# Optimization experiments

Measured on AMD Instinct MI355X. Metric: run time of the kernel, lower is better.

Reference implementation:

```python
import jax, jax.numpy as jnp
import numpy as np

COMMITMENT_COST = 0.25
NUM_EMBEDDINGS = 1024
EMBEDDING_DIM = 256


def setup_inputs() -> dict:
    key = jax.random.key(0)
    k1, k2 = jax.random.split(key)
    inputs = jax.random.normal(k1, (16, 4096, EMBEDDING_DIM), dtype=jnp.float32)
    # codebook initialized uniform(-1/K, 1/K) as in the torch module
    embeddings = jax.random.uniform(
        k2, (NUM_EMBEDDINGS, EMBEDDING_DIM), dtype=jnp.float32,
        minval=-1.0 / NUM_EMBEDDINGS, maxval=1.0 / NUM_EMBEDDINGS)
    return {"inputs": inputs, "embeddings": embeddings}


def reference(inputs, embeddings):
    sg = jax.lax.stop_gradient
    D = embeddings.shape[1]
    input_shape = inputs.shape
    flat = sg(inputs).reshape(-1, D)  # [N, D]
    distances = (jnp.sum(embeddings ** 2, axis=1)
                 + jnp.sum(flat ** 2, axis=1, keepdims=True)
                 - 2.0 * jnp.matmul(flat, embeddings.T))  # [N, K]
    indices = jnp.argmin(distances, axis=-1)  # [N]
    quantized = embeddings[indices].reshape(input_shape)
    e_latent_loss = jnp.mean((sg(quantized) - inputs) ** 2)
    q_latent_loss = jnp.mean((quantized - sg(inputs)) ** 2)
    loss = q_latent_loss + COMMITMENT_COST * e_latent_loss
    # straight-through estimator
    quantized = inputs + sg(quantized - inputs)
    return loss, quantized
```

## Files before the change

### kernel.cpp

```cpp
#include <hip/hip_runtime.h>
#include <math.h>

#define DIM 256
#define KCODES 1024
#define NTILE 64
#define BM 128
#define ESCALE 512.0f
#define UNIT_SCALE 0x7F7F7F7F

typedef __attribute__((ext_vector_type(8))) int i32x8;
typedef __attribute__((ext_vector_type(4))) float f32x4;

__global__ __launch_bounds__(64) void vq_prep_kernel(
    const float* __restrict__ E, float* __restrict__ enormh,
    unsigned char* __restrict__ Ef8) {
  const int k = blockIdx.x;
  const int t = threadIdx.x;
  const float4 v = *reinterpret_cast<const float4*>(&E[k * DIM + t * 4]);
  const int d0 = t * 4;
  const size_t byte = (size_t)((k >> 4) * 4096) + (size_t)((d0 >> 7) * 2048) +
                      (size_t)(((((d0 >> 5) & 3) * 16) + (k & 15)) * 32) +
                      (size_t)(d0 & 31);
  int p = __builtin_amdgcn_cvt_pk_fp8_f32(v.x * ESCALE, v.y * ESCALE, 0, 0);
  p = __builtin_amdgcn_cvt_pk_fp8_f32(v.z * ESCALE, v.w * ESCALE, p, 1);
  *reinterpret_cast<unsigned int*>(Ef8 + byte) = (unsigned int)p;
  float s = v.x * v.x + v.y * v.y + v.z * v.z + v.w * v.w;
#pragma unroll
  for (int off = 32; off >= 1; off >>= 1) s += __shfl_down(s, off);
  if (t == 0) enormh[k] = -0.5f * ESCALE * s;
}

__global__ __launch_bounds__(256, 2) void vq_fused_kernel(
    const float* __restrict__ X, const float* __restrict__ E,
    const unsigned char* __restrict__ Ef8, const float* __restrict__ enormh,
    float* __restrict__ outq, float* __restrict__ partials) {
  __shared__ __attribute__((aligned(16))) char ring[4][4][4096];
  __shared__ float enorm_s[KCODES];
  __shared__ int idxs[BM];
  __shared__ float lred[4];

  const int tid = threadIdx.x;
  const int w = tid >> 6;
  const int lane = tid & 63;
  const int lr = lane & 15;
  const int lk = lane >> 4;
  const int row0 = blockIdx.x * BM;

  {
    const float4 v = *reinterpret_cast<const float4*>(&enormh[tid * 4]);
    *reinterpret_cast<float4*>(&enorm_s[tid * 4]) = v;
  }

  i32x8 Af[2][2];
  float xsq = 0.0f;
#pragma unroll
  for (int mt = 0; mt < 2; ++mt) {
    const float* xrow = &X[(size_t)(row0 + w * 32 + mt * 16 + lr) * DIM];
#pragma unroll
    for (int ks2 = 0; ks2 < 2; ++ks2) {
      const int k0 = ks2 * 128 + lk * 32;
      i32x8 af;
#pragma unroll
      for (int p = 0; p < 8; ++p) {
        const float4 a = *reinterpret_cast<const float4*>(&xrow[k0 + p * 4]);
        xsq += a.x * a.x + a.y * a.y + a.z * a.z + a.w * a.w;
        int pk = __builtin_amdgcn_cvt_pk_fp8_f32(a.x, a.y, 0, 0);
        pk = __builtin_amdgcn_cvt_pk_fp8_f32(a.z, a.w, pk, 1);
        af[p] = pk;
      }
      Af[mt][ks2] = af;
    }
  }

  float maxv[8];
  int mini[8];
#pragma unroll
  for (int i = 0; i < 8; ++i) { maxv[i] = -INFINITY; mini[i] = 0; }

  const char* efsrc = reinterpret_cast<const char*>(Ef8) + lane * 16;
  char* ringw = &ring[w][0][0];

  __syncthreads();

#define ISSUE(T)                                                              \
  {                                                                           \
    const char* src_ = efsrc + (size_t)(T) * 4096;                            \
    char* dst_ = ringw + ((T) & 3) * 4096;                                    \
    _Pragma("unroll") for (int i_ = 0; i_ < 4; ++i_)                          \
        __builtin_amdgcn_global_load_lds(                                     \
            (const __attribute__((address_space(1))) unsigned int*)(src_ +    \
                                                                    i_ *      \
                                                                        1024),\
            (__attribute__((address_space(3))) unsigned int*)(dst_ +          \
                                                              i_ * 1024 +     \
                                                              lane * 16),     \
            16, 0, 0);                                                        \
  }

#define CONSUME(T)                                                            \
  {                                                                           \
    const char* cbuf_ = ringw + ((T) & 3) * 4096;                             \
    const float en_ = enorm_s[(T) * 16 + lr];                                 \
    const i32x8 b0_ = *reinterpret_cast<const i32x8*>(cbuf_ + lane * 32);     \
    const i32x8 b1_ =                                                         \
        *reinterpret_cast<const i32x8*>(cbuf_ + 2048 + lane * 32);            \
    f32x4 acc0, acc1;                                                         \
    acc0[0] = en_; acc0[1] = en_; acc0[2] = en_; acc0[3] = en_;               \
    acc1 = acc0;                                                              \
    acc0 = __builtin_amdgcn_mfma_scale_f32_16x16x128_f8f6f4(                  \
        Af[0][0], b0_, acc0, 0, 0, 0, UNIT_SCALE, 0, UNIT_SCALE);             \
    acc1 = __builtin_amdgcn_mfma_scale_f32_16x16x128_f8f6f4(                  \
        Af[1][0], b0_, acc1, 0, 0, 0, UNIT_SCALE, 0, UNIT_SCALE);             \
    acc0 = __builtin_amdgcn_mfma_scale_f32_16x16x128_f8f6f4(                  \
        Af[0][1], b1_, acc0, 0, 0, 0, UNIT_SCALE, 0, UNIT_SCALE);             \
    acc1 = __builtin_amdgcn_mfma_scale_f32_16x16x128_f8f6f4(                  \
        Af[1][1], b1_, acc1, 0, 0, 0, UNIT_SCALE, 0, UNIT_SCALE);             \
    const int code_ = (T) * 16 + lr;                                          \
    _Pragma("unroll") for (int r_ = 0; r_ < 4; ++r_) {                        \
      if (acc0[r_] > maxv[r_]) { maxv[r_] = acc0[r_]; mini[r_] = code_; }     \
      if (acc1[r_] > maxv[4 + r_]) {                                          \
        maxv[4 + r_] = acc1[r_]; mini[4 + r_] = code_;                        \
      }                                                                       \
    }                                                                         \
  }

  ISSUE(0);
  ISSUE(1);
  ISSUE(2);

#pragma unroll 4
  for (int t = 0; t < NTILE - 4; ++t) {
    ISSUE(t + 3);
    asm volatile("s_waitcnt vmcnt(12)" ::: "memory");
    __builtin_amdgcn_sched_barrier(0);
    CONSUME(t);
  }
  ISSUE(63);
  asm volatile("s_waitcnt vmcnt(12)" ::: "memory");
  __builtin_amdgcn_sched_barrier(0);
  CONSUME(60);
  asm volatile("s_waitcnt vmcnt(8)" ::: "memory");
  __builtin_amdgcn_sched_barrier(0);
  CONSUME(61);
  asm volatile("s_waitcnt vmcnt(4)" ::: "memory");
  __builtin_amdgcn_sched_barrier(0);
  CONSUME(62);
  asm volatile("s_waitcnt vmcnt(0)" ::: "memory");
  __builtin_amdgcn_sched_barrier(0);
  CONSUME(63);
#undef ISSUE
#undef CONSUME

#pragma unroll
  for (int off = 1; off < 16; off <<= 1) {
#pragma unroll
    for (int ri = 0; ri < 8; ++ri) {
      const float ov = __shfl_xor(maxv[ri], off);
      const int oi = __shfl_xor(mini[ri], off);
      if (ov > maxv[ri] || (ov == maxv[ri] && oi < mini[ri])) {
        maxv[ri] = ov; mini[ri] = oi;
      }
    }
  }
  if (lr == 0) {
#pragma unroll
    for (int mt = 0; mt < 2; ++mt)
#pragma unroll
      for (int r = 0; r < 4; ++r)
        idxs[w * 32 + mt * 16 + lk * 4 + r] = mini[mt * 4 + r];
  }

  float lsum = xsq;
  if (lr == 0) {
    float ssum = 0.0f;
#pragma unroll
    for (int ri = 0; ri < 8; ++ri) ssum += maxv[ri];
    lsum += ssum * (-2.0f / ESCALE);
  }
#pragma unroll
  for (int off = 32; off >= 1; off >>= 1) lsum += __shfl_down(lsum, off);
  if (lane == 0) lred[w] = lsum;
  __syncthreads();

#pragma unroll
  for (int half = 0; half < 2; ++half) {
    const int er = half * 64 + (tid >> 2);
    const int eq = tid & 3;
    const int code = idxs[er];
    const float* erow = &E[(size_t)code * DIM];
    float* orow = &outq[(size_t)(row0 + er) * DIM];
#pragma unroll
    for (int j = 0; j < 16; ++j) {
      const int d = j * 16 + eq * 4;
      *reinterpret_cast<float4*>(&orow[d]) =
          *reinterpret_cast<const float4*>(&erow[d]);
    }
  }
  if (tid == 0)
    partials[blockIdx.x] = lred[0] + lred[1] + lred[2] + lred[3];
}

__global__ __launch_bounds__(256) void vq_finalize_kernel(
    const float* __restrict__ partials, float* __restrict__ out_loss,
    int nparts, float inv_count) {
  const int tid = threadIdx.x;
  float s = 0.0f;
  for (int i = tid; i < nparts; i += 256) s += partials[i];
#pragma unroll
  for (int off = 32; off >= 1; off >>= 1) s += __shfl_down(s, off);
  __shared__ float w[4];
  if ((tid & 63) == 0) w[tid >> 6] = s;
  __syncthreads();
  if (tid == 0)
    out_loss[0] = 1.25f * (w[0] + w[1] + w[2] + w[3]) * inv_count;
}

extern "C" void kernel_launch(void* const* d_in, const int* in_sizes, int n_in,
                              void* d_out, int out_size, void* d_ws,
                              size_t ws_size, hipStream_t stream) {
  const float* X = (const float*)d_in[0];
  const float* E = (const float*)d_in[1];
  float* out = (float*)d_out;

  char* ws = (char*)d_ws;
  float* enormh = (float*)ws;
  float* partials = (float*)(ws + 16 * 1024);
  unsigned char* Ef8 = (unsigned char*)(ws + 48 * 1024);

  const int nrows = in_sizes[0] / DIM;
  const int nb_main = nrows / BM;

  vq_prep_kernel<<<KCODES, 64, 0, stream>>>(E, enormh, Ef8);
  vq_fused_kernel<<<nb_main, 256, 0, stream>>>(X, E, Ef8, enormh, out + 1,
                                               partials);
  vq_finalize_kernel<<<1, 256, 0, stream>>>(partials, out, nb_main,
                                            1.0f / (float)in_sizes[0]);
}
```

Measured before the change: 62.94 us.

## Load fp8 codebook tiles directly into registers instead of LDS ring

Drops the per-wave LDS ring buffer fed by global_load_lds and the shared enorm copy. The pre-swizzled fp8 codebook tiles and norms are now loaded straight from global (L2) into registers, double-buffered two tiles ahead, inside a fully unrolled loop. This removes LDS traffic, the block barrier and the manual waitcnt choreography, and frees LDS for higher occupancy. The cost is more VGPRs and reliance on the compiler's waitcnt placement to hide global latency with only two tiles of prefetch.

```diff
diff --git a/kernel.cpp b/kernel.cpp
--- a/kernel.cpp
+++ b/kernel.cpp
@@ -34,8 +34,6 @@
     const float* __restrict__ X, const float* __restrict__ E,
     const unsigned char* __restrict__ Ef8, const float* __restrict__ enormh,
     float* __restrict__ outq, float* __restrict__ partials) {
-  __shared__ __attribute__((aligned(16))) char ring[4][4][4096];
-  __shared__ float enorm_s[KCODES];
   __shared__ int idxs[BM];
   __shared__ float lred[4];
 
@@ -45,11 +43,6 @@
   const int lr = lane & 15;
   const int lk = lane >> 4;
   const int row0 = blockIdx.x * BM;
-
-  {
-    const float4 v = *reinterpret_cast<const float4*>(&enormh[tid * 4]);
-    *reinterpret_cast<float4*>(&enorm_s[tid * 4]) = v;
-  }
 
   i32x8 Af[2][2];
   float xsq = 0.0f;
@@ -77,79 +70,60 @@
 #pragma unroll
   for (int i = 0; i < 8; ++i) { maxv[i] = -INFINITY; mini[i] = 0; }
 
-  const char* efsrc = reinterpret_cast<const char*>(Ef8) + lane * 16;
-  char* ringw = &ring[w][0][0];
-
-  __syncthreads();
-
-#define ISSUE(T)                                                              \
+  const char* efbase = reinterpret_cast<const char*>(Ef8) + lane * 32;
+
+  i32x8 B0a, B0b, B1a, B1b;
+  float en0, en1;
+  B0a = *reinterpret_cast<const i32x8*>(efbase);
+  B0b = *reinterpret_cast<const i32x8*>(efbase + 2048);
+  B1a = *reinterpret_cast<const i32x8*>(efbase + 4096);
+  B1b = *reinterpret_cast<const i32x8*>(efbase + 4096 + 2048);
+  en0 = enormh[lr];
+  en1 = enormh[16 + lr];
+
+#define COMPUTE_TILE(BA, BB)                                                  \
   {                                                                           \
-    const char* src_ = efsrc + (size_t)(T) * 4096;                            \
-    char* dst_ = ringw + ((T) & 3) * 4096;                                    \
-    _Pragma("unroll") for (int i_ = 0; i_ < 4; ++i_)                          \
-        __builtin_amdgcn_global_load_lds(                                     \
-            (const __attribute__((address_space(1))) unsigned int*)(src_ +    \
-                                                                    i_ *      \
-                                                                        1024),\
-            (__attribute__((address_space(3))) unsigned int*)(dst_ +          \
-                                                              i_ * 1024 +     \
-                                                              lane * 16),     \
-            16, 0, 0);                                                        \
-  }
-
-#define CONSUME(T)                                                            \
+    acc0 = __builtin_amdgcn_mfma_scale_f32_16x16x128_f8f6f4(                  \
+        Af[0][0], BA, acc0, 0, 0, 0, UNIT_SCALE, 0, UNIT_SCALE);              \
+    acc1 = __builtin_amdgcn_mfma_scale_f32_16x16x128_f8f6f4(                  \
+        Af[1][0], BA, acc1, 0, 0, 0, UNIT_SCALE, 0, UNIT_SCALE);              \
+    acc0 = __builtin_amdgcn_mfma_scale_f32_16x16x128_f8f6f4(                  \
+        Af[0][1], BB, acc0, 0, 0, 0, UNIT_SCALE, 0, UNIT_SCALE);              \
+    acc1 = __builtin_amdgcn_mfma_scale_f32_16x16x128_f8f6f4(                  \
+        Af[1][1], BB, acc1, 0, 0, 0, UNIT_SCALE, 0, UNIT_SCALE);              \
+  }
+
+#define RELOAD(BA, BB, EN, TILE)                                              \
   {                                                                           \
-    const char* cbuf_ = ringw + ((T) & 3) * 4096;                             \
-    const float en_ = enorm_s[(T) * 16 + lr];                                 \
-    const i32x8 b0_ = *reinterpret_cast<const i32x8*>(cbuf_ + lane * 32);     \
-    const i32x8 b1_ =                                                         \
-        *reinterpret_cast<const i32x8*>(cbuf_ + 2048 + lane * 32);            \
-    f32x4 acc0, acc1;                                                         \
-    acc0[0] = en_; acc0[1] = en_; acc0[2] = en_; acc0[3] = en_;               \
-    acc1 = acc0;                                                              \
-    acc0 = __builtin_amdgcn_mfma_scale_f32_16x16x128_f8f6f4(                  \
-        Af[0][0], b0_, acc0, 0, 0, 0, UNIT_SCALE, 0, UNIT_SCALE);             \
-    acc1 = __builtin_amdgcn_mfma_scale_f32_16x16x128_f8f6f4(                  \
-        Af[1][0], b0_, acc1, 0, 0, 0, UNIT_SCALE, 0, UNIT_SCALE);             \
-    acc0 = __builtin_amdgcn_mfma_scale_f32_16x16x128_f8f6f4(                  \
-        Af[0][1], b1_, acc0, 0, 0, 0, UNIT_SCALE, 0, UNIT_SCALE);             \
-    acc1 = __builtin_amdgcn_mfma_scale_f32_16x16x128_f8f6f4(                  \
-        Af[1][1], b1_, acc1, 0, 0, 0, UNIT_SCALE, 0, UNIT_SCALE);             \
-    const int code_ = (T) * 16 + lr;                                          \
-    _Pragma("unroll") for (int r_ = 0; r_ < 4; ++r_) {                        \
-      if (acc0[r_] > maxv[r_]) { maxv[r_] = acc0[r_]; mini[r_] = code_; }     \
-      if (acc1[r_] > maxv[4 + r_]) {                                          \
-        maxv[4 + r_] = acc1[r_]; mini[4 + r_] = code_;                        \
-      }                                                                       \
-    }                                                                         \
-  }
-
-  ISSUE(0);
-  ISSUE(1);
-  ISSUE(2);
-
-#pragma unroll 4
-  for (int t = 0; t < NTILE - 4; ++t) {
-    ISSUE(t + 3);
-    asm volatile("s_waitcnt vmcnt(12)" ::: "memory");
-    __builtin_amdgcn_sched_barrier(0);
-    CONSUME(t);
-  }
-  ISSUE(63);
-  asm volatile("s_waitcnt vmcnt(12)" ::: "memory");
-  __builtin_amdgcn_sched_barrier(0);
-  CONSUME(60);
-  asm volatile("s_waitcnt vmcnt(8)" ::: "memory");
-  __builtin_amdgcn_sched_barrier(0);
-  CONSUME(61);
-  asm volatile("s_waitcnt vmcnt(4)" ::: "memory");
-  __builtin_amdgcn_sched_barrier(0);
-  CONSUME(62);
-  asm volatile("s_waitcnt vmcnt(0)" ::: "memory");
-  __builtin_amdgcn_sched_barrier(0);
-  CONSUME(63);
-#undef ISSUE
-#undef CONSUME
+    const char* nsrc = efbase + (size_t)(TILE) * 4096;                        \
+    BA = *reinterpret_cast<const i32x8*>(nsrc);                               \
+    BB = *reinterpret_cast<const i32x8*>(nsrc + 2048);                        \
+    EN = enormh[(TILE) * 16 + lr];                                            \
+  }
+
+#pragma unroll
+  for (int t = 0; t < NTILE; ++t) {
+    f32x4 acc0, acc1;
+    if (t & 1) {
+      acc0[0] = en1; acc0[1] = en1; acc0[2] = en1; acc0[3] = en1;
+      acc1 = acc0;
+      COMPUTE_TILE(B1a, B1b);
+      if (t + 2 < NTILE) RELOAD(B1a, B1b, en1, t + 2);
+    } else {
+      acc0[0] = en0; acc0[1] = en0; acc0[2] = en0; acc0[3] = en0;
+      acc1 = acc0;
+      COMPUTE_TILE(B0a, B0b);
+      if (t + 2 < NTILE) RELOAD(B0a, B0b, en0, t + 2);
+    }
+    const int code = t * 16 + lr;
+#pragma unroll
+    for (int r = 0; r < 4; ++r) {
+      if (acc0[r] > maxv[r]) { maxv[r] = acc0[r]; mini[r] = code; }
+      if (acc1[r] > maxv[4 + r]) { maxv[4 + r] = acc1[r]; mini[4 + r] = code; }
+    }
+  }
+#undef COMPUTE_TILE
+#undef RELOAD
 
 #pragma unroll
   for (int off = 1; off < 16; off <<= 1) {
```

Result: faster. 55.01 us (-12.6%).
